# Kernel optimization log

Measured on AMD Instinct MI355X. Metric: run time of the kernel, lower is better.

Reference implementation:

```python
import jax, jax.numpy as jnp
import numpy as np

EPS = 1e-12
BETA = 0.25

def normalise(x, axis=-1):
    return x * jax.lax.rsqrt(jnp.mean(x * x, axis=axis, keepdims=True) + EPS)

def setup_inputs() -> dict:
    key = jax.random.key(0)
    ks = jax.random.split(key, 4)
    N, F, D, C = 8192, 512, 64, 8192
    return {
        "z": jax.random.normal(ks[0], (N, F), dtype=jnp.float32),
        "W_in": jax.random.normal(ks[1], (F, D), dtype=jnp.float32) * (1.0 / np.sqrt(F)),
        "b_in": jnp.zeros((D,), dtype=jnp.float32),
        "codebook": jax.random.normal(ks[2], (C, D), dtype=jnp.float32),
        "W_out": jax.random.normal(ks[3], (D, F), dtype=jnp.float32) * (1.0 / np.sqrt(D)),
        "b_out": jnp.zeros((F,), dtype=jnp.float32),
    }

def reference(z, W_in, b_in, codebook, W_out, b_out):
    sg = jax.lax.stop_gradient
    # input projection: [N, F] -> [N, D]
    zp = z @ W_in + b_in
    zn = normalise(zp)                  # [N, D]
    cn = normalise(codebook)            # [C, D]
    # squared euclidean distance via matmul expansion (same math as
    # sum((z[:,None]-c[None])**2, -1), avoids [N,C,D] materialization)
    z_sq = jnp.sum(zn * zn, axis=-1, keepdims=True)          # [N, 1]
    c_sq = jnp.sum(cn * cn, axis=-1)[None, :]                # [1, C]
    distance = z_sq + c_sq - 2.0 * (zn @ cn.T)               # [N, C]
    idxes = jnp.argmin(distance, axis=-1)                    # [N]
    codes = normalise(codebook[idxes], axis=-1)               # [N, D]
    loss = BETA * jnp.mean((sg(zn) - codes) ** 2) + jnp.mean((zn - sg(codes)) ** 2)
    codes = zn + sg(codes - zn)                               # straight-through
    out = codes @ W_out + b_out                               # [N, F]
    return (out, loss, idxes)
```

## Files before the change

### kernel.cpp

```cpp
#include <hip/hip_runtime.h>
#include <hip/hip_bf16.h>

#define N_ROWS 8192
#define F_DIM  512
#define D_DIM  64
#define C_CODES 8192

typedef __attribute__((ext_vector_type(8))) short bf16x8;
typedef __attribute__((ext_vector_type(4))) float f32x4;

__device__ __forceinline__ unsigned short rne_bf16(float x) {
  unsigned u = __float_as_uint(x);
  return (unsigned short)((u + 0x7FFFu + ((u >> 16) & 1u)) >> 16);
}
__device__ __forceinline__ float bf16_to_f(unsigned short u) {
  return __uint_as_float(((unsigned)u) << 16);
}
__device__ __forceinline__ void limb3(const float* xs, bf16x8& H, bf16x8& M, bf16x8& L) {
  #pragma unroll
  for (int j = 0; j < 8; ++j) {
    float x = xs[j];
    unsigned short h = rne_bf16(x);
    float r1 = x - bf16_to_f(h);
    unsigned short m = rne_bf16(r1);
    float r2 = r1 - bf16_to_f(m);
    unsigned short lo = rne_bf16(r2);
    H[j] = (short)h; M[j] = (short)m; L[j] = (short)lo;
  }
}

__global__ __launch_bounds__(256) void k_swz_win(
    const float* __restrict__ W, unsigned short* __restrict__ dst) {
  const int tid = threadIdx.x, w = tid >> 6, l = tid & 63;
  const int task = blockIdx.x * 4 + w;
  const int kc = task >> 2, cg = task & 3;
  const int lo = l & 15, hi = l >> 4;
  float xs[8];
  #pragma unroll
  for (int j = 0; j < 8; ++j)
    xs[j] = W[(size_t)(kc * 32 + hi * 8 + j) * D_DIM + cg * 16 + lo];
  bf16x8 H, M, L;
  limb3(xs, H, M, L);
  const int fb = (kc * 4 + cg) * 3;
  unsigned short* d0 = dst + (size_t)(fb + 0) * 512 + l * 8;
  unsigned short* d1 = dst + (size_t)(fb + 1) * 512 + l * 8;
  unsigned short* d2 = dst + (size_t)(fb + 2) * 512 + l * 8;
  #pragma unroll
  for (int j = 0; j < 8; ++j) { d0[j] = (unsigned short)H[j]; d1[j] = (unsigned short)M[j]; d2[j] = (unsigned short)L[j]; }
}

__global__ __launch_bounds__(256) void k_swz_wout(
    const float* __restrict__ W, unsigned short* __restrict__ dst) {
  const int tid = threadIdx.x, w = tid >> 6, l = tid & 63;
  const int task = blockIdx.x * 4 + w;
  const int cg = task >> 1, c = task & 1;
  const int lo = l & 15, hi = l >> 4;
  float xs[8];
  #pragma unroll
  for (int j = 0; j < 8; ++j)
    xs[j] = W[(size_t)(c * 32 + hi * 8 + j) * F_DIM + cg * 16 + lo];
  bf16x8 H, M, L;
  limb3(xs, H, M, L);
  const int fb = (cg * 2 + c) * 3;
  unsigned short* d0 = dst + (size_t)(fb + 0) * 512 + l * 8;
  unsigned short* d1 = dst + (size_t)(fb + 1) * 512 + l * 8;
  unsigned short* d2 = dst + (size_t)(fb + 2) * 512 + l * 8;
  #pragma unroll
  for (int j = 0; j < 8; ++j) { d0[j] = (unsigned short)H[j]; d1[j] = (unsigned short)M[j]; d2[j] = (unsigned short)L[j]; }
}

__global__ __launch_bounds__(256) void k_cn(
    const float* __restrict__ cb, float* __restrict__ cn,
    unsigned short* __restrict__ cn_sw) {
  const int tid = threadIdx.x, w = tid >> 6, l = tid & 63;
  const int g = blockIdx.x * 4 + w;
  const int lo = l & 15, hi = l >> 4;
  const int code = g * 16 + lo;

  float xs[2][8];
  float s = 0.0f;
  #pragma unroll
  for (int c = 0; c < 2; ++c) {
    const float* sp = cb + (size_t)code * D_DIM + c * 32 + hi * 8;
    float4 a = *(const float4*)sp, b = *(const float4*)(sp + 4);
    xs[c][0]=a.x; xs[c][1]=a.y; xs[c][2]=a.z; xs[c][3]=a.w;
    xs[c][4]=b.x; xs[c][5]=b.y; xs[c][6]=b.z; xs[c][7]=b.w;
    #pragma unroll
    for (int j = 0; j < 8; ++j) s += xs[c][j] * xs[c][j];
  }
  s += __shfl_xor(s, 16);
  s += __shfl_xor(s, 32);
  float inv = rsqrtf(s * (1.0f / 64.0f) + 1e-12f);

  #pragma unroll
  for (int c = 0; c < 2; ++c) {
    #pragma unroll
    for (int j = 0; j < 8; ++j) xs[c][j] *= inv;
    float* dp = cn + (size_t)code * D_DIM + c * 32 + hi * 8;
    *(float4*)dp = make_float4(xs[c][0], xs[c][1], xs[c][2], xs[c][3]);
    *(float4*)(dp + 4) = make_float4(xs[c][4], xs[c][5], xs[c][6], xs[c][7]);
    bf16x8 H, M, L;
    limb3(xs[c], H, M, L);
    const int fb = (g * 2 + c) * 3;
    unsigned short* d0 = cn_sw + (size_t)(fb + 0) * 512 + l * 8;
    unsigned short* d1 = cn_sw + (size_t)(fb + 1) * 512 + l * 8;
    unsigned short* d2 = cn_sw + (size_t)(fb + 2) * 512 + l * 8;
    #pragma unroll
    for (int j = 0; j < 8; ++j) { d0[j] = (unsigned short)H[j]; d1[j] = (unsigned short)M[j]; d2[j] = (unsigned short)L[j]; }
  }
}

__global__ __launch_bounds__(64) void k_zn(
    const float* __restrict__ z, const unsigned short* __restrict__ w_in_sw,
    const float* __restrict__ b_in, float* __restrict__ zn,
    unsigned short* __restrict__ zn_sw) {
  __shared__ float t_lds[16 * 65];
  const int l = threadIdx.x;
  const int lo = l & 15, hi = l >> 4;
  const int g = blockIdx.x;
  const int r0 = g * 16;
  const bf16x8* Bptr = (const bf16x8*)w_in_sw;
  const float* zbase = z + (size_t)(r0 + lo) * F_DIM + hi * 8;

  f32x4 acc[4];
  #pragma unroll
  for (int cg = 0; cg < 4; ++cg) acc[cg] = (f32x4){0.f, 0.f, 0.f, 0.f};

  bf16x8 Bu[12], Bv[12];
  #pragma unroll
  for (int i = 0; i < 12; ++i) Bu[i] = Bptr[(size_t)i * 64 + l];
  float4 za = *(const float4*)zbase;
  float4 zb = *(const float4*)(zbase + 4);

  #define ZSTEP(BCUR, BNXT, KC)                                               \
    {                                                                         \
      int kn = ((KC) < 15) ? (KC) + 1 : 15;                                   \
      float4 na = *(const float4*)(zbase + kn * 32);                          \
      float4 nb = *(const float4*)(zbase + kn * 32 + 4);                      \
      _Pragma("unroll")                                                       \
      for (int i = 0; i < 12; ++i)                                            \
        BNXT[i] = Bptr[((size_t)kn * 12 + i) * 64 + l];                       \
      float xs[8] = {za.x, za.y, za.z, za.w, zb.x, zb.y, zb.z, zb.w};         \
      bf16x8 Ah, Am, Al;                                                      \
      limb3(xs, Ah, Am, Al);                                                  \
      _Pragma("unroll")                                                       \
      for (int cg = 0; cg < 4; ++cg) {                                        \
        f32x4 t = acc[cg];                                                    \
        t = __builtin_amdgcn_mfma_f32_16x16x32_bf16(Ah, BCUR[cg*3+0], t, 0,0,0); \
        t = __builtin_amdgcn_mfma_f32_16x16x32_bf16(Ah, BCUR[cg*3+1], t, 0,0,0); \
        t = __builtin_amdgcn_mfma_f32_16x16x32_bf16(Am, BCUR[cg*3+0], t, 0,0,0); \
        t = __builtin_amdgcn_mfma_f32_16x16x32_bf16(Ah, BCUR[cg*3+2], t, 0,0,0); \
        t = __builtin_amdgcn_mfma_f32_16x16x32_bf16(Al, BCUR[cg*3+0], t, 0,0,0); \
        t = __builtin_amdgcn_mfma_f32_16x16x32_bf16(Am, BCUR[cg*3+1], t, 0,0,0); \
        acc[cg] = t;                                                          \
      }                                                                       \
      za = na; zb = nb;                                                       \
    }

  for (int kc = 0; kc < 16; kc += 2) {
    ZSTEP(Bu, Bv, kc)
    ZSTEP(Bv, Bu, kc + 1)
  }
  #undef ZSTEP

  #pragma unroll
  for (int r = 0; r < 4; ++r) {
    float v[4], s = 0.0f;
    #pragma unroll
    for (int cg = 0; cg < 4; ++cg) {
      v[cg] = acc[cg][r] + b_in[cg * 16 + lo];
      s += v[cg] * v[cg];
    }
    s += __shfl_xor(s, 1);
    s += __shfl_xor(s, 2);
    s += __shfl_xor(s, 4);
    s += __shfl_xor(s, 8);
    float inv = rsqrtf(s * (1.0f / 64.0f) + 1e-12f);
    #pragma unroll
    for (int cg = 0; cg < 4; ++cg)
      t_lds[(hi * 4 + r) * 65 + cg * 16 + lo] = v[cg] * inv;
  }
  __syncthreads();

  #pragma unroll
  for (int c = 0; c < 2; ++c) {
    float xs[8];
    #pragma unroll
    for (int j = 0; j < 8; ++j) xs[j] = t_lds[lo * 65 + c * 32 + hi * 8 + j];
    float* dp = zn + (size_t)(r0 + lo) * D_DIM + c * 32 + hi * 8;
    *(float4*)dp = make_float4(xs[0], xs[1], xs[2], xs[3]);
    *(float4*)(dp + 4) = make_float4(xs[4], xs[5], xs[6], xs[7]);
    bf16x8 H, M, L;
    limb3(xs, H, M, L);
    const int fb = (g * 2 + c) * 3;
    unsigned short* d0 = zn_sw + (size_t)(fb + 0) * 512 + l * 8;
    unsigned short* d1 = zn_sw + (size_t)(fb + 1) * 512 + l * 8;
    unsigned short* d2 = zn_sw + (size_t)(fb + 2) * 512 + l * 8;
    #pragma unroll
    for (int j = 0; j < 8; ++j) { d0[j] = (unsigned short)H[j]; d1[j] = (unsigned short)M[j]; d2[j] = (unsigned short)L[j]; }
  }
}

__global__ __launch_bounds__(256, 2) void k_argmax(
    const unsigned short* __restrict__ zn_sw,
    const unsigned short* __restrict__ cn_sw,
    float* __restrict__ pval, int* __restrict__ pidx) {
  const int tid = threadIdx.x;
  const int w = tid >> 6, l = tid & 63;
  const int lo = l & 15, hi = l >> 4;
  const int gA0 = (blockIdx.x * 4 + w) * 2;
  const int gB0 = blockIdx.y * 64;
  const bf16x8* Ab = (const bf16x8*)zn_sw;
  const bf16x8* Bb = (const bf16x8*)cn_sw;

  bf16x8 A0[2][3], A1[2][3];
  #pragma unroll
  for (int c = 0; c < 2; ++c)
    #pragma unroll
    for (int m = 0; m < 3; ++m) {
      A0[c][m] = Ab[(size_t)((gA0 * 2 + c) * 3 + m) * 64 + l];
      A1[c][m] = Ab[(size_t)(((gA0 + 1) * 2 + c) * 3 + m) * 64 + l];
    }

  bf16x8 Bu[2][3], Bv[2][3];
  #pragma unroll
  for (int c = 0; c < 2; ++c)
    #pragma unroll
    for (int m = 0; m < 3; ++m)
      Bu[c][m] = Bb[(size_t)((gB0 * 2 + c) * 3 + m) * 64 + l];

  float bv[8];
  int bi[8];
  #pragma unroll
  for (int i = 0; i < 8; ++i) { bv[i] = -1e30f; bi[i] = 0; }
  int cand = blockIdx.y * 1024 + lo;

  #define LOADB(dst, gB)                                                     \
    _Pragma("unroll")                                                        \
    for (int c = 0; c < 2; ++c)                                              \
      _Pragma("unroll")                                                      \
      for (int m = 0; m < 3; ++m)                                            \
        dst[c][m] = Bb[(size_t)(((gB) * 2 + c) * 3 + m) * 64 + l];

  #define COMPUTE(B)                                                          \
    {                                                                         \
      f32x4 a0 = {0.f,0.f,0.f,0.f}, a1 = {0.f,0.f,0.f,0.f};                   \
      f32x4 a2 = {0.f,0.f,0.f,0.f}, a3 = {0.f,0.f,0.f,0.f};                   \
      a0 = __builtin_amdgcn_mfma_f32_16x16x32_bf16(A0[0][0], B[0][0], a0, 0,0,0); \
      a1 = __builtin_amdgcn_mfma_f32_16x16x32_bf16(A0[1][0], B[1][0], a1, 0,0,0); \
      a2 = __builtin_amdgcn_mfma_f32_16x16x32_bf16(A1[0][0], B[0][0], a2, 0,0,0); \
      a3 = __builtin_amdgcn_mfma_f32_16x16x32_bf16(A1[1][0], B[1][0], a3, 0,0,0); \
      a0 = __builtin_amdgcn_mfma_f32_16x16x32_bf16(A0[0][0], B[0][1], a0, 0,0,0); \
      a1 = __builtin_amdgcn_mfma_f32_16x16x32_bf16(A0[1][0], B[1][1], a1, 0,0,0); \
      a2 = __builtin_amdgcn_mfma_f32_16x16x32_bf16(A1[0][0], B[0][1], a2, 0,0,0); \
      a3 = __builtin_amdgcn_mfma_f32_16x16x32_bf16(A1[1][0], B[1][1], a3, 0,0,0); \
      a0 = __builtin_amdgcn_mfma_f32_16x16x32_bf16(A0[0][1], B[0][0], a0, 0,0,0); \
      a1 = __builtin_amdgcn_mfma_f32_16x16x32_bf16(A0[1][1], B[1][0], a1, 0,0,0); \
      a2 = __builtin_amdgcn_mfma_f32_16x16x32_bf16(A1[0][1], B[0][0], a2, 0,0,0); \
      a3 = __builtin_amdgcn_mfma_f32_16x16x32_bf16(A1[1][1], B[1][0], a3, 0,0,0); \
      a0 = __builtin_amdgcn_mfma_f32_16x16x32_bf16(A0[0][0], B[0][2], a0, 0,0,0); \
      a1 = __builtin_amdgcn_mfma_f32_16x16x32_bf16(A0[1][0], B[1][2], a1, 0,0,0); \
      a2 = __builtin_amdgcn_mfma_f32_16x16x32_bf16(A1[0][0], B[0][2], a2, 0,0,0); \
      a3 = __builtin_amdgcn_mfma_f32_16x16x32_bf16(A1[1][0], B[1][2], a3, 0,0,0); \
      a0 = __builtin_amdgcn_mfma_f32_16x16x32_bf16(A0[0][2], B[0][0], a0, 0,0,0); \
      a1 = __builtin_amdgcn_mfma_f32_16x16x32_bf16(A0[1][2], B[1][0], a1, 0,0,0); \
      a2 = __builtin_amdgcn_mfma_f32_16x16x32_bf16(A1[0][2], B[0][0], a2, 0,0,0); \
      a3 = __builtin_amdgcn_mfma_f32_16x16x32_bf16(A1[1][2], B[1][0], a3, 0,0,0); \
      a0 = __builtin_amdgcn_mfma_f32_16x16x32_bf16(A0[0][1], B[0][1], a0, 0,0,0); \
      a1 = __builtin_amdgcn_mfma_f32_16x16x32_bf16(A0[1][1], B[1][1], a1, 0,0,0); \
      a2 = __builtin_amdgcn_mfma_f32_16x16x32_bf16(A1[0][1], B[0][1], a2, 0,0,0); \
      a3 = __builtin_amdgcn_mfma_f32_16x16x32_bf16(A1[1][1], B[1][1], a3, 0,0,0); \
      _Pragma("unroll")                                                       \
      for (int r = 0; r < 4; ++r) {                                           \
        float d0 = a0[r] + a1[r];                                             \
        if (d0 > bv[r]) { bv[r] = d0; bi[r] = cand; }                         \
        float d1 = a2[r] + a3[r];                                             \
        if (d1 > bv[4 + r]) { bv[4 + r] = d1; bi[4 + r] = cand; }             \
      }                                                                       \
      cand += 16;                                                             \
    }

  for (int p = 0; p < 64; p += 2) {
    LOADB(Bv, gB0 + p + 1);
    COMPUTE(Bu);
    LOADB(Bu, gB0 + p + 2);
    COMPUTE(Bv);
  }
  #undef LOADB
  #undef COMPUTE

  #pragma unroll
  for (int i = 0; i < 8; ++i) {
    float v = bv[i]; int ix = bi[i];
    #pragma unroll
    for (int m = 1; m < 16; m <<= 1) {
      float ov = __shfl_xor(v, m);
      int oi = __shfl_xor(ix, m);
      if (ov > v || (ov == v && oi < ix)) { v = ov; ix = oi; }
    }
    bv[i] = v; bi[i] = ix;
  }
  if (lo == 0) {
    int off = blockIdx.y * N_ROWS;
    int base0 = gA0 * 16 + hi * 4;
    int base1 = (gA0 + 1) * 16 + hi * 4;
    #pragma unroll
    for (int r = 0; r < 4; ++r) {
      pval[off + base0 + r] = bv[r];     pidx[off + base0 + r] = bi[r];
      pval[off + base1 + r] = bv[4 + r]; pidx[off + base1 + r] = bi[4 + r];
    }
  }
}

__global__ __launch_bounds__(64) void k_out(
    const float* __restrict__ cn, const float* __restrict__ zn,
    const float* __restrict__ pval, const int* __restrict__ pidx,
    const unsigned short* __restrict__ w_out_sw,
    const float* __restrict__ b_out, float* __restrict__ out,
    float* __restrict__ idx_f, float* __restrict__ pl) {
  const int l = threadIdx.x;
  const int lo = l & 15, hi = l >> 4;
  const int r0 = blockIdx.x * 16;
  const int row = r0 + lo;

  float v = pval[row];
  int ix = pidx[row];
  #pragma unroll
  for (int q = 1; q < 8; ++q) {
    float vq = pval[q * N_ROWS + row];
    int iq = pidx[q * N_ROWS + row];
    if (vq > v) { v = vq; ix = iq; }
  }
  if (hi == 0) idx_f[row] = (float)ix;

  bf16x8 A[2][3];
  float lp = 0.0f;
  #pragma unroll
  for (int c = 0; c < 2; ++c) {
    const float* cp = cn + (size_t)ix * D_DIM + c * 32 + hi * 8;
    const float* zp = zn + (size_t)row * D_DIM + c * 32 + hi * 8;
    float4 c0 = *(const float4*)cp, c1 = *(const float4*)(cp + 4);
    float4 z0 = *(const float4*)zp, z1 = *(const float4*)(zp + 4);
    float xs[8] = {c0.x, c0.y, c0.z, c0.w, c1.x, c1.y, c1.z, c1.w};
    float zs[8] = {z0.x, z0.y, z0.z, z0.w, z1.x, z1.y, z1.z, z1.w};
    limb3(xs, A[c][0], A[c][1], A[c][2]);
    #pragma unroll
    for (int j = 0; j < 8; ++j) { float d = xs[j] - zs[j]; lp += d * d; }
  }
  #pragma unroll
  for (int m = 1; m < 64; m <<= 1) lp += __shfl_xor(lp, m);
  if (l == 0) pl[blockIdx.x] = lp;

  const bf16x8* Bptr = (const bf16x8*)w_out_sw;
  bf16x8 Bu[6], Bv[6];
  #pragma unroll
  for (int i = 0; i < 6; ++i) Bu[i] = Bptr[(size_t)i * 64 + l];

  #define OSTEP(BCUR, BNXT, CG)                                               \
    {                                                                         \
      _Pragma("unroll")                                                       \
      for (int i = 0; i < 6; ++i)                                             \
        BNXT[i] = Bptr[((size_t)((CG) + 1) * 6 + i) * 64 + l];                \
      f32x4 a0 = {0.f,0.f,0.f,0.f}, a1 = {0.f,0.f,0.f,0.f};                   \
      a0 = __builtin_amdgcn_mfma_f32_16x16x32_bf16(A[0][0], BCUR[0], a0, 0,0,0); \
      a1 = __builtin_amdgcn_mfma_f32_16x16x32_bf16(A[1][0], BCUR[3], a1, 0,0,0); \
      a0 = __builtin_amdgcn_mfma_f32_16x16x32_bf16(A[0][0], BCUR[1], a0, 0,0,0); \
      a1 = __builtin_amdgcn_mfma_f32_16x16x32_bf16(A[1][0], BCUR[4], a1, 0,0,0); \
      a0 = __builtin_amdgcn_mfma_f32_16x16x32_bf16(A[0][1], BCUR[0], a0, 0,0,0); \
      a1 = __builtin_amdgcn_mfma_f32_16x16x32_bf16(A[1][1], BCUR[3], a1, 0,0,0); \
      a0 = __builtin_amdgcn_mfma_f32_16x16x32_bf16(A[0][0], BCUR[2], a0, 0,0,0); \
      a1 = __builtin_amdgcn_mfma_f32_16x16x32_bf16(A[1][0], BCUR[5], a1, 0,0,0); \
      a0 = __builtin_amdgcn_mfma_f32_16x16x32_bf16(A[0][2], BCUR[0], a0, 0,0,0); \
      a1 = __builtin_amdgcn_mfma_f32_16x16x32_bf16(A[1][2], BCUR[3], a1, 0,0,0); \
      a0 = __builtin_amdgcn_mfma_f32_16x16x32_bf16(A[0][1], BCUR[1], a0, 0,0,0); \
      a1 = __builtin_amdgcn_mfma_f32_16x16x32_bf16(A[1][1], BCUR[4], a1, 0,0,0); \
      float bb = b_out[(CG) * 16 + lo];                                       \
      _Pragma("unroll")                                                       \
      for (int r = 0; r < 4; ++r)                                             \
        out[(size_t)(r0 + hi * 4 + r) * F_DIM + (CG) * 16 + lo] =             \
            a0[r] + a1[r] + bb;                                               \
    }

  for (int cg = 0; cg < 32; cg += 2) {
    OSTEP(Bu, Bv, cg)
    OSTEP(Bv, Bu, cg + 1)
  }
  #undef OSTEP
}

__global__ __launch_bounds__(64) void k_loss_final(
    const float* __restrict__ pl, float* __restrict__ loss_out) {
  const int l = threadIdx.x;
  float s = 0.0f;
  #pragma unroll
  for (int i = 0; i < 8; ++i) s += pl[l + 64 * i];
  #pragma unroll
  for (int m = 1; m < 64; m <<= 1) s += __shfl_xor(s, m);
  if (l == 0) loss_out[0] = s * (1.25f / (float)(N_ROWS * D_DIM));
}

extern "C" void kernel_launch(void* const* d_in, const int* in_sizes, int n_in,
                              void* d_out, int out_size, void* d_ws, size_t ws_size,
                              hipStream_t stream) {
  const float* z        = (const float*)d_in[0];
  const float* W_in     = (const float*)d_in[1];
  const float* b_in     = (const float*)d_in[2];
  const float* codebook = (const float*)d_in[3];
  const float* W_out    = (const float*)d_in[4];
  const float* b_out    = (const float*)d_in[5];

  float* outp   = (float*)d_out;
  float* loss_f = outp + (size_t)N_ROWS * F_DIM;
  float* idx_f  = loss_f + 1;

  float* wsf = (float*)d_ws;
  float* zn_ws = wsf;
  float* cn_ws = wsf + 524288;
  unsigned short* zn_sw = (unsigned short*)(wsf + 1048576);
  unsigned short* cn_sw = (unsigned short*)(wsf + 1835008);
  unsigned short* win_sw  = (unsigned short*)(wsf + 2625536);
  unsigned short* wout_sw = (unsigned short*)(wsf + 2674688);
  float* pval_ws = wsf + 2723840;
  int*   pidx_ws = (int*)(wsf + 2789376);
  float* pl_ws   = wsf + 2854912;

  hipLaunchKernelGGL(k_swz_win, dim3(16), dim3(256), 0, stream, W_in, win_sw);
  hipLaunchKernelGGL(k_swz_wout, dim3(16), dim3(256), 0, stream, W_out, wout_sw);
  hipLaunchKernelGGL(k_cn, dim3(128), dim3(256), 0, stream,
                     codebook, cn_ws, cn_sw);
  hipLaunchKernelGGL(k_zn, dim3(512), dim3(64), 0, stream,
                     z, win_sw, b_in, zn_ws, zn_sw);
  hipLaunchKernelGGL(k_argmax, dim3(64, 8), dim3(256), 0, stream,
                     zn_sw, cn_sw, pval_ws, pidx_ws);
  hipLaunchKernelGGL(k_out, dim3(512), dim3(64), 0, stream,
                     cn_ws, zn_ws, pval_ws, pidx_ws, wout_sw, b_out,
                     outp, idx_f, pl_ws);
  hipLaunchKernelGGL(k_loss_final, dim3(1), dim3(64), 0, stream,
                     pl_ws, loss_f);
}
```

Measured before the change: 154.8 us.

## Merge prep kernels, deepen load prefetching, and replace loss-final kernel with atomics

Three preprocessing kernels (W_in swizzle, W_out swizzle, codebook normalise) are merged into one launch with block-range dispatch. The final loss-reduction kernel is removed: k_zn zeroes the loss and k_out accumulates scaled partials with atomicAdd. The z loads in k_zn are prefetched four chunks ahead, and the codebook and W_out operand loads in k_argmax and k_out become triple-buffered. The aim is fewer launches and better hiding of global-load latency, at the cost of more registers and non-deterministic float atomic ordering for the loss.

```diff
diff --git a/kernel.cpp b/kernel.cpp
--- a/kernel.cpp
+++ b/kernel.cpp
@@ -29,96 +29,91 @@
   }
 }
 
-__global__ __launch_bounds__(256) void k_swz_win(
-    const float* __restrict__ W, unsigned short* __restrict__ dst) {
+__global__ __launch_bounds__(256) void k_prep(
+    const float* __restrict__ W_in, const float* __restrict__ W_out,
+    const float* __restrict__ cb,
+    unsigned short* __restrict__ win_sw, unsigned short* __restrict__ wout_sw,
+    float* __restrict__ cn, unsigned short* __restrict__ cn_sw) {
+  const int b = blockIdx.x;
   const int tid = threadIdx.x, w = tid >> 6, l = tid & 63;
-  const int task = blockIdx.x * 4 + w;
-  const int kc = task >> 2, cg = task & 3;
   const int lo = l & 15, hi = l >> 4;
-  float xs[8];
-  #pragma unroll
-  for (int j = 0; j < 8; ++j)
-    xs[j] = W[(size_t)(kc * 32 + hi * 8 + j) * D_DIM + cg * 16 + lo];
-  bf16x8 H, M, L;
-  limb3(xs, H, M, L);
-  const int fb = (kc * 4 + cg) * 3;
-  unsigned short* d0 = dst + (size_t)(fb + 0) * 512 + l * 8;
-  unsigned short* d1 = dst + (size_t)(fb + 1) * 512 + l * 8;
-  unsigned short* d2 = dst + (size_t)(fb + 2) * 512 + l * 8;
-  #pragma unroll
-  for (int j = 0; j < 8; ++j) { d0[j] = (unsigned short)H[j]; d1[j] = (unsigned short)M[j]; d2[j] = (unsigned short)L[j]; }
-}
-
-__global__ __launch_bounds__(256) void k_swz_wout(
-    const float* __restrict__ W, unsigned short* __restrict__ dst) {
-  const int tid = threadIdx.x, w = tid >> 6, l = tid & 63;
-  const int task = blockIdx.x * 4 + w;
-  const int cg = task >> 1, c = task & 1;
-  const int lo = l & 15, hi = l >> 4;
-  float xs[8];
-  #pragma unroll
-  for (int j = 0; j < 8; ++j)
-    xs[j] = W[(size_t)(c * 32 + hi * 8 + j) * F_DIM + cg * 16 + lo];
-  bf16x8 H, M, L;
-  limb3(xs, H, M, L);
-  const int fb = (cg * 2 + c) * 3;
-  unsigned short* d0 = dst + (size_t)(fb + 0) * 512 + l * 8;
-  unsigned short* d1 = dst + (size_t)(fb + 1) * 512 + l * 8;
-  unsigned short* d2 = dst + (size_t)(fb + 2) * 512 + l * 8;
-  #pragma unroll
-  for (int j = 0; j < 8; ++j) { d0[j] = (unsigned short)H[j]; d1[j] = (unsigned short)M[j]; d2[j] = (unsigned short)L[j]; }
-}
-
-__global__ __launch_bounds__(256) void k_cn(
-    const float* __restrict__ cb, float* __restrict__ cn,
-    unsigned short* __restrict__ cn_sw) {
-  const int tid = threadIdx.x, w = tid >> 6, l = tid & 63;
-  const int g = blockIdx.x * 4 + w;
-  const int lo = l & 15, hi = l >> 4;
-  const int code = g * 16 + lo;
-
-  float xs[2][8];
-  float s = 0.0f;
-  #pragma unroll
-  for (int c = 0; c < 2; ++c) {
-    const float* sp = cb + (size_t)code * D_DIM + c * 32 + hi * 8;
-    float4 a = *(const float4*)sp, b = *(const float4*)(sp + 4);
-    xs[c][0]=a.x; xs[c][1]=a.y; xs[c][2]=a.z; xs[c][3]=a.w;
-    xs[c][4]=b.x; xs[c][5]=b.y; xs[c][6]=b.z; xs[c][7]=b.w;
-    #pragma unroll
-    for (int j = 0; j < 8; ++j) s += xs[c][j] * xs[c][j];
-  }
-  s += __shfl_xor(s, 16);
-  s += __shfl_xor(s, 32);
-  float inv = rsqrtf(s * (1.0f / 64.0f) + 1e-12f);
-
-  #pragma unroll
-  for (int c = 0; c < 2; ++c) {
-    #pragma unroll
-    for (int j = 0; j < 8; ++j) xs[c][j] *= inv;
-    float* dp = cn + (size_t)code * D_DIM + c * 32 + hi * 8;
-    *(float4*)dp = make_float4(xs[c][0], xs[c][1], xs[c][2], xs[c][3]);
-    *(float4*)(dp + 4) = make_float4(xs[c][4], xs[c][5], xs[c][6], xs[c][7]);
+
+  if (b < 16) {
+    const int task = b * 4 + w;
+    const int kc = task >> 2, cg = task & 3;
+    float xs[8];
+    #pragma unroll
+    for (int j = 0; j < 8; ++j)
+      xs[j] = W_in[(size_t)(kc * 32 + hi * 8 + j) * D_DIM + cg * 16 + lo];
     bf16x8 H, M, L;
-    limb3(xs[c], H, M, L);
-    const int fb = (g * 2 + c) * 3;
-    unsigned short* d0 = cn_sw + (size_t)(fb + 0) * 512 + l * 8;
-    unsigned short* d1 = cn_sw + (size_t)(fb + 1) * 512 + l * 8;
-    unsigned short* d2 = cn_sw + (size_t)(fb + 2) * 512 + l * 8;
+    limb3(xs, H, M, L);
+    const int fb = (kc * 4 + cg) * 3;
+    unsigned short* d0 = win_sw + (size_t)(fb + 0) * 512 + l * 8;
+    unsigned short* d1 = win_sw + (size_t)(fb + 1) * 512 + l * 8;
+    unsigned short* d2 = win_sw + (size_t)(fb + 2) * 512 + l * 8;
     #pragma unroll
     for (int j = 0; j < 8; ++j) { d0[j] = (unsigned short)H[j]; d1[j] = (unsigned short)M[j]; d2[j] = (unsigned short)L[j]; }
+  } else if (b < 32) {
+    const int task = (b - 16) * 4 + w;
+    const int cg = task >> 1, c = task & 1;
+    float xs[8];
+    #pragma unroll
+    for (int j = 0; j < 8; ++j)
+      xs[j] = W_out[(size_t)(c * 32 + hi * 8 + j) * F_DIM + cg * 16 + lo];
+    bf16x8 H, M, L;
+    limb3(xs, H, M, L);
+    const int fb = (cg * 2 + c) * 3;
+    unsigned short* d0 = wout_sw + (size_t)(fb + 0) * 512 + l * 8;
+    unsigned short* d1 = wout_sw + (size_t)(fb + 1) * 512 + l * 8;
+    unsigned short* d2 = wout_sw + (size_t)(fb + 2) * 512 + l * 8;
+    #pragma unroll
+    for (int j = 0; j < 8; ++j) { d0[j] = (unsigned short)H[j]; d1[j] = (unsigned short)M[j]; d2[j] = (unsigned short)L[j]; }
+  } else {
+    const int g = (b - 32) * 4 + w;
+    const int code = g * 16 + lo;
+    float xs[2][8];
+    float s = 0.0f;
+    #pragma unroll
+    for (int c = 0; c < 2; ++c) {
+      const float* sp = cb + (size_t)code * D_DIM + c * 32 + hi * 8;
+      float4 a = *(const float4*)sp, bb = *(const float4*)(sp + 4);
+      xs[c][0]=a.x; xs[c][1]=a.y; xs[c][2]=a.z; xs[c][3]=a.w;
+      xs[c][4]=bb.x; xs[c][5]=bb.y; xs[c][6]=bb.z; xs[c][7]=bb.w;
+      #pragma unroll
+      for (int j = 0; j < 8; ++j) s += xs[c][j] * xs[c][j];
+    }
+    s += __shfl_xor(s, 16);
+    s += __shfl_xor(s, 32);
+    float inv = rsqrtf(s * (1.0f / 64.0f) + 1e-12f);
+    #pragma unroll
+    for (int c = 0; c < 2; ++c) {
+      #pragma unroll
+      for (int j = 0; j < 8; ++j) xs[c][j] *= inv;
+      float* dp = cn + (size_t)code * D_DIM + c * 32 + hi * 8;
+      *(float4*)dp = make_float4(xs[c][0], xs[c][1], xs[c][2], xs[c][3]);
+      *(float4*)(dp + 4) = make_float4(xs[c][4], xs[c][5], xs[c][6], xs[c][7]);
+      bf16x8 H, M, L;
+      limb3(xs[c], H, M, L);
+      const int fb = (g * 2 + c) * 3;
+      unsigned short* d0 = cn_sw + (size_t)(fb + 0) * 512 + l * 8;
+      unsigned short* d1 = cn_sw + (size_t)(fb + 1) * 512 + l * 8;
+      unsigned short* d2 = cn_sw + (size_t)(fb + 2) * 512 + l * 8;
+      #pragma unroll
+      for (int j = 0; j < 8; ++j) { d0[j] = (unsigned short)H[j]; d1[j] = (unsigned short)M[j]; d2[j] = (unsigned short)L[j]; }
+    }
   }
 }
 
 __global__ __launch_bounds__(64) void k_zn(
     const float* __restrict__ z, const unsigned short* __restrict__ w_in_sw,
     const float* __restrict__ b_in, float* __restrict__ zn,
-    unsigned short* __restrict__ zn_sw) {
+    unsigned short* __restrict__ zn_sw, float* __restrict__ loss_zero) {
   __shared__ float t_lds[16 * 65];
   const int l = threadIdx.x;
   const int lo = l & 15, hi = l >> 4;
   const int g = blockIdx.x;
   const int r0 = g * 16;
+  if (g == 0 && l == 0) loss_zero[0] = 0.0f;
   const bf16x8* Bptr = (const bf16x8*)w_in_sw;
   const float* zbase = z + (size_t)(r0 + lo) * F_DIM + hi * 8;
 
@@ -126,42 +121,46 @@
   #pragma unroll
   for (int cg = 0; cg < 4; ++cg) acc[cg] = (f32x4){0.f, 0.f, 0.f, 0.f};
 
-  bf16x8 Bu[12], Bv[12];
-  #pragma unroll
-  for (int i = 0; i < 12; ++i) Bu[i] = Bptr[(size_t)i * 64 + l];
-  float4 za = *(const float4*)zbase;
-  float4 zb = *(const float4*)(zbase + 4);
-
-  #define ZSTEP(BCUR, BNXT, KC)                                               \
-    {                                                                         \
-      int kn = ((KC) < 15) ? (KC) + 1 : 15;                                   \
-      float4 na = *(const float4*)(zbase + kn * 32);                          \
-      float4 nb = *(const float4*)(zbase + kn * 32 + 4);                      \
-      _Pragma("unroll")                                                       \
-      for (int i = 0; i < 12; ++i)                                            \
-        BNXT[i] = Bptr[((size_t)kn * 12 + i) * 64 + l];                       \
-      float xs[8] = {za.x, za.y, za.z, za.w, zb.x, zb.y, zb.z, zb.w};         \
-      bf16x8 Ah, Am, Al;                                                      \
-      limb3(xs, Ah, Am, Al);                                                  \
-      _Pragma("unroll")                                                       \
-      for (int cg = 0; cg < 4; ++cg) {                                        \
-        f32x4 t = acc[cg];                                                    \
-        t = __builtin_amdgcn_mfma_f32_16x16x32_bf16(Ah, BCUR[cg*3+0], t, 0,0,0); \
-        t = __builtin_amdgcn_mfma_f32_16x16x32_bf16(Ah, BCUR[cg*3+1], t, 0,0,0); \
-        t = __builtin_amdgcn_mfma_f32_16x16x32_bf16(Am, BCUR[cg*3+0], t, 0,0,0); \
-        t = __builtin_amdgcn_mfma_f32_16x16x32_bf16(Ah, BCUR[cg*3+2], t, 0,0,0); \
-        t = __builtin_amdgcn_mfma_f32_16x16x32_bf16(Al, BCUR[cg*3+0], t, 0,0,0); \
-        t = __builtin_amdgcn_mfma_f32_16x16x32_bf16(Am, BCUR[cg*3+1], t, 0,0,0); \
-        acc[cg] = t;                                                          \
-      }                                                                       \
-      za = na; zb = nb;                                                       \
-    }
-
-  for (int kc = 0; kc < 16; kc += 2) {
-    ZSTEP(Bu, Bv, kc)
-    ZSTEP(Bv, Bu, kc + 1)
-  }
-  #undef ZSTEP
+  bf16x8 Bpp[2][12];
+  float4 zq[4][2];
+  #pragma unroll
+  for (int i = 0; i < 4; ++i) {
+    zq[i][0] = *(const float4*)(zbase + i * 32);
+    zq[i][1] = *(const float4*)(zbase + i * 32 + 4);
+  }
+  #pragma unroll
+  for (int i = 0; i < 12; ++i) Bpp[0][i] = Bptr[(size_t)i * 64 + l];
+
+  #pragma unroll
+  for (int kc = 0; kc < 16; ++kc) {
+    float4 na, nb;
+    const bool hz = (kc + 4 < 16);
+    if (hz) {
+      na = *(const float4*)(zbase + (kc + 4) * 32);
+      nb = *(const float4*)(zbase + (kc + 4) * 32 + 4);
+    }
+    if (kc + 1 < 16) {
+      #pragma unroll
+      for (int i = 0; i < 12; ++i)
+        Bpp[(kc + 1) & 1][i] = Bptr[((size_t)(kc + 1) * 12 + i) * 64 + l];
+    }
+    float xs[8] = {zq[kc & 3][0].x, zq[kc & 3][0].y, zq[kc & 3][0].z, zq[kc & 3][0].w,
+                   zq[kc & 3][1].x, zq[kc & 3][1].y, zq[kc & 3][1].z, zq[kc & 3][1].w};
+    bf16x8 Ah, Am, Al;
+    limb3(xs, Ah, Am, Al);
+    #pragma unroll
+    for (int cg = 0; cg < 4; ++cg) {
+      f32x4 t = acc[cg];
+      t = __builtin_amdgcn_mfma_f32_16x16x32_bf16(Ah, Bpp[kc & 1][cg*3+0], t, 0,0,0);
+      t = __builtin_amdgcn_mfma_f32_16x16x32_bf16(Ah, Bpp[kc & 1][cg*3+1], t, 0,0,0);
+      t = __builtin_amdgcn_mfma_f32_16x16x32_bf16(Am, Bpp[kc & 1][cg*3+0], t, 0,0,0);
+      t = __builtin_amdgcn_mfma_f32_16x16x32_bf16(Ah, Bpp[kc & 1][cg*3+2], t, 0,0,0);
+      t = __builtin_amdgcn_mfma_f32_16x16x32_bf16(Al, Bpp[kc & 1][cg*3+0], t, 0,0,0);
+      t = __builtin_amdgcn_mfma_f32_16x16x32_bf16(Am, Bpp[kc & 1][cg*3+1], t, 0,0,0);
+      acc[cg] = t;
+    }
+    if (hz) { zq[kc & 3][0] = na; zq[kc & 3][1] = nb; }
+  }
 
   #pragma unroll
   for (int r = 0; r < 4; ++r) {
@@ -221,13 +220,6 @@
       A0[c][m] = Ab[(size_t)((gA0 * 2 + c) * 3 + m) * 64 + l];
       A1[c][m] = Ab[(size_t)(((gA0 + 1) * 2 + c) * 3 + m) * 64 + l];
     }
-
-  bf16x8 Bu[2][3], Bv[2][3];
-  #pragma unroll
-  for (int c = 0; c < 2; ++c)
-    #pragma unroll
-    for (int m = 0; m < 3; ++m)
-      Bu[c][m] = Bb[(size_t)((gB0 * 2 + c) * 3 + m) * 64 + l];
 
   float bv[8];
   int bi[8];
@@ -280,12 +272,18 @@
       cand += 16;                                                             \
     }
 
-  for (int p = 0; p < 64; p += 2) {
-    LOADB(Bv, gB0 + p + 1);
-    COMPUTE(Bu);
-    LOADB(Bu, gB0 + p + 2);
-    COMPUTE(Bv);
-  }
+  bf16x8 B0v[2][3], B1v[2][3], B2v[2][3];
+  LOADB(B0v, gB0);
+  LOADB(B1v, gB0 + 1);
+  for (int p = 0; p + 3 <= 64; p += 3) {
+    LOADB(B2v, gB0 + p + 2);
+    COMPUTE(B0v);
+    LOADB(B0v, gB0 + p + 3);
+    COMPUTE(B1v);
+    LOADB(B1v, gB0 + p + 4);
+    COMPUTE(B2v);
+  }
+  COMPUTE(B0v);
   #undef LOADB
   #undef COMPUTE
 
@@ -317,7 +315,7 @@
     const float* __restrict__ pval, const int* __restrict__ pidx,
     const unsigned short* __restrict__ w_out_sw,
     const float* __restrict__ b_out, float* __restrict__ out,
-    float* __restrict__ idx_f, float* __restrict__ pl) {
+    float* __restrict__ idx_f, float* __restrict__ loss_f) {
   const int l = threadIdx.x;
   const int lo = l & 15, hi = l >> 4;
   const int r0 = blockIdx.x * 16;
@@ -349,18 +347,17 @@
   }
   #pragma unroll
   for (int m = 1; m < 64; m <<= 1) lp += __shfl_xor(lp, m);
-  if (l == 0) pl[blockIdx.x] = lp;
+  if (l == 0) atomicAdd(loss_f, lp * (1.25f / (float)(N_ROWS * D_DIM)));
 
   const bf16x8* Bptr = (const bf16x8*)w_out_sw;
-  bf16x8 Bu[6], Bv[6];
-  #pragma unroll
-  for (int i = 0; i < 6; ++i) Bu[i] = Bptr[(size_t)i * 64 + l];
-
-  #define OSTEP(BCUR, BNXT, CG)                                               \
+
+  #define LOADW(dst, CG)                                                      \
+    _Pragma("unroll")                                                         \
+    for (int i = 0; i < 6; ++i)                                               \
+      dst[i] = Bptr[((size_t)(CG) * 6 + i) * 64 + l];
+
+  #define OSTEP(BCUR, CG)                                                     \
     {                                                                         \
-      _Pragma("unroll")                                                       \
-      for (int i = 0; i < 6; ++i)                                             \
-        BNXT[i] = Bptr[((size_t)((CG) + 1) * 6 + i) * 64 + l];                \
       f32x4 a0 = {0.f,0.f,0.f,0.f}, a1 = {0.f,0.f,0.f,0.f};                   \
       a0 = __builtin_amdgcn_mfma_f32_16x16x32_bf16(A[0][0], BCUR[0], a0, 0,0,0); \
       a1 = __builtin_amdgcn_mfma_f32_16x16x32_bf16(A[1][0], BCUR[3], a1, 0,0,0); \
@@ -381,22 +378,21 @@
             a0[r] + a1[r] + bb;                                               \
     }
 
-  for (int cg = 0; cg < 32; cg += 2) {
-    OSTEP(Bu, Bv, cg)
-    OSTEP(Bv, Bu, cg + 1)
-  }
+  bf16x8 B0v[6], B1v[6], B2v[6];
+  LOADW(B0v, 0);
+  LOADW(B1v, 1);
+  for (int cg = 0; cg + 3 <= 32; cg += 3) {
+    LOADW(B2v, cg + 2);
+    OSTEP(B0v, cg);
+    LOADW(B0v, cg + 3);
+    OSTEP(B1v, cg + 1);
+    LOADW(B1v, cg + 4);
+    OSTEP(B2v, cg + 2);
+  }
+  OSTEP(B0v, 30);
+  OSTEP(B1v, 31);
+  #undef LOADW
   #undef OSTEP
-}
-
-__global__ __launch_bounds__(64) void k_loss_final(
-    const float* __restrict__ pl, float* __restrict__ loss_out) {
-  const int l = threadIdx.x;
-  float s = 0.0f;
-  #pragma unroll
-  for (int i = 0; i < 8; ++i) s += pl[l + 64 * i];
-  #pragma unroll
-  for (int m = 1; m < 64; m <<= 1) s += __shfl_xor(s, m);
-  if (l == 0) loss_out[0] = s * (1.25f / (float)(N_ROWS * D_DIM));
 }
 
 extern "C" void kernel_launch(void* const* d_in, const int* in_sizes, int n_in,
@@ -422,19 +418,14 @@
   unsigned short* wout_sw = (unsigned short*)(wsf + 2674688);
   float* pval_ws = wsf + 2723840;
   int*   pidx_ws = (int*)(wsf + 2789376);
-  float* pl_ws   = wsf + 2854912;
-
-  hipLaunchKernelGGL(k_swz_win, dim3(16), dim3(256), 0, stream, W_in, win_sw);
-  hipLaunchKernelGGL(k_swz_wout, dim3(16), dim3(256), 0, stream, W_out, wout_sw);
-  hipLaunchKernelGGL(k_cn, dim3(128), dim3(256), 0, stream,
-                     codebook, cn_ws, cn_sw);
+
+  hipLaunchKernelGGL(k_prep, dim3(160), dim3(256), 0, stream,
+                     W_in, W_out, codebook, win_sw, wout_sw, cn_ws, cn_sw);
   hipLaunchKernelGGL(k_zn, dim3(512), dim3(64), 0, stream,
-                     z, win_sw, b_in, zn_ws, zn_sw);
+                     z, win_sw, b_in, zn_ws, zn_sw, loss_f);
   hipLaunchKernelGGL(k_argmax, dim3(64, 8), dim3(256), 0, stream,
                      zn_sw, cn_sw, pval_ws, pidx_ws);
   hipLaunchKernelGGL(k_out, dim3(512), dim3(64), 0, stream,
                      cn_ws, zn_ws, pval_ws, pidx_ws, wout_sw, b_out,
-                     outp, idx_f, pl_ws);
-  hipLaunchKernelGGL(k_loss_final, dim3(1), dim3(64), 0, stream,
-                     pl_ws, loss_f);
-}
+                     outp, idx_f, loss_f);
+}
```

Measured after the change: 175.1 us. 1.13x slower.
